# Optimization experiments

Hardware: AMD Instinct MI355X
Metric: run time of the kernel (lower is better)

## Reference

```python
import jax, jax.numpy as jnp
import numpy as np

N, E = 50000, 800000
IN, MID, OUT = 128, 256, 128
LN_EPS = 1e-5


def layer_norm(x, gamma, beta, eps=LN_EPS):
    mu = jnp.mean(x, axis=-1, keepdims=True)
    var = jnp.mean(jnp.square(x - mu), axis=-1, keepdims=True)
    return (x - mu) * jax.lax.rsqrt(var + eps) * gamma + beta


def gcn_conv(x, W, b, src, dst, norm, n):
    # x' = D^{-1/2}(A+I)D^{-1/2} X W + b  (self-loops already folded into src/dst/norm)
    h = x @ W                                  # [N, F_out]
    msg = h[src] * norm[:, None]               # [E+N, F_out] gather + scale
    out = jax.ops.segment_sum(msg, dst, num_segments=n)
    return out + b


def setup_inputs() -> dict:
    key = jax.random.key(0)
    ks = jax.random.split(key, 4)
    x = jax.random.normal(ks[0], (N, IN), dtype=jnp.float32)
    edge_index = jax.random.randint(ks[1], (2, E), 0, N, dtype=jnp.int32)
    W1 = jax.random.normal(ks[2], (IN, MID), dtype=jnp.float32) * (1.0 / np.sqrt(IN))
    b1 = jnp.zeros((MID,), jnp.float32)
    g1 = jnp.ones((IN,), jnp.float32)
    be1 = jnp.zeros((IN,), jnp.float32)
    W4 = jax.random.normal(ks[3], (MID, OUT), dtype=jnp.float32) * (1.0 / np.sqrt(MID))
    b4 = jnp.zeros((OUT,), jnp.float32)
    g4 = jnp.ones((MID,), jnp.float32)
    be4 = jnp.zeros((MID,), jnp.float32)
    return {"x": x, "W1": W1, "b1": b1, "g1": g1, "be1": be1,
            "W4": W4, "b4": b4, "g4": g4, "be4": be4,
            "edge_index": edge_index}


def reference(x, W1, b1, g1, be1, W4, b4, g4, be4, edge_index):
    n = x.shape[0]
    loop = jnp.arange(n, dtype=edge_index.dtype)
    src = jnp.concatenate([edge_index[0], loop])   # [E+N]
    dst = jnp.concatenate([edge_index[1], loop])   # [E+N]
    deg = jax.ops.segment_sum(jnp.ones_like(src, x.dtype), dst, num_segments=n)
    dinv = jax.lax.rsqrt(deg)                      # deg >= 1 thanks to self-loops
    norm = dinv[src] * dinv[dst]                   # [E+N]

    h = gcn_conv(layer_norm(x, g1, be1), W1, b1, src, dst, norm, n)
    h = jax.nn.gelu(h, approximate=False)          # torch F.gelu default = exact erf
    h = gcn_conv(layer_norm(h, g4, be4), W4, b4, src, dst, norm, n)
    return h
```

## Files before the change

### kernel.cpp

```cpp
#include <hip/hip_runtime.h>
#include <math.h>

#define N_NODES 50000
#define E_EDGES 800000

typedef __attribute__((ext_vector_type(4))) float f32x4;
typedef __attribute__((ext_vector_type(8))) short s16x8;

#define T1_OFF    0UL
#define AGG1_OFF  12800000UL
#define T2B_OFF   38400000UL
#define WB1H_OFF  64000000UL
#define WB1L_OFF  64100096UL
#define WB4H_OFF  64200192UL
#define WB4L_OFF  64300288UL
#define DINV_OFF  64400384UL
#define HIST_OFF  64600576UL
#define RP_OFF    64800768UL
#define CUR_OFF   65001088UL
#define CSR_OFF   65201408UL
#define BSUM_OFF  71601408UL

__device__ __forceinline__ float lo16f(unsigned u) { return __uint_as_float(u << 16); }
__device__ __forceinline__ float hi16f(unsigned u) { return __uint_as_float(u & 0xffff0000u); }
__device__ __forceinline__ unsigned pack2bf(float a, float b) {
  unsigned ua = __float_as_uint(a); ua += 0x7fffu + ((ua >> 16) & 1u);
  unsigned ub = __float_as_uint(b); ub += 0x7fffu + ((ub >> 16) & 1u);
  return (ua >> 16) | (ub & 0xffff0000u);
}
__device__ __forceinline__ float gelu_f(float x) {
  return 0.5f * x * (1.f + erff(x * 0.70710678118654752f));
}

__global__ __launch_bounds__(256) void init_hist(int* __restrict__ hist, int n) {
  int i = blockIdx.x * 256 + threadIdx.x;
  if (i < n) hist[i] = 0;
}

__global__ __launch_bounds__(256) void hist_kernel(const int* __restrict__ dst,
                                                   int* __restrict__ hist, int e) {
  int i = blockIdx.x * 256 + threadIdx.x;
  if (i < e) atomicAdd(&hist[dst[i]], 1);
}

__global__ __launch_bounds__(256) void dinv_kernel(const int* __restrict__ hist,
                                                   float* __restrict__ dinv, int n) {
  int i = blockIdx.x * 256 + threadIdx.x;
  if (i < n) dinv[i] = rsqrtf((float)(hist[i] + 1));
}

__global__ __launch_bounds__(1024) void scan_partial(const int* __restrict__ hist,
                                                     int* __restrict__ rp,
                                                     int* __restrict__ bsum, int n) {
  __shared__ int wsum[16];
  int tid = threadIdx.x, lane = tid & 63, wv = tid >> 6;
  int i = blockIdx.x * 1024 + tid;
  int v = (i < n) ? hist[i] : 0;
  int sc = v;
  #pragma unroll
  for (int m = 1; m < 64; m <<= 1) { int o = __shfl_up(sc, m); if (lane >= m) sc += o; }
  if (lane == 63) wsum[wv] = sc;
  __syncthreads();
  if (wv == 0) {
    int w = (lane < 16) ? wsum[lane] : 0;
    int swc = w;
    #pragma unroll
    for (int m = 1; m < 16; m <<= 1) { int o = __shfl_up(swc, m); if (lane >= m) swc += o; }
    if (lane < 16) wsum[lane] = swc - w;
    if (lane == 15) bsum[blockIdx.x] = swc;
  }
  __syncthreads();
  if (i < n) rp[i] = (sc - v) + wsum[wv];
}

__global__ __launch_bounds__(64) void scan_bsums(int* __restrict__ bsum, int nb) {
  int lane = threadIdx.x;
  int v = (lane < nb) ? bsum[lane] : 0;
  int sc = v;
  #pragma unroll
  for (int m = 1; m < 64; m <<= 1) { int o = __shfl_up(sc, m); if (lane >= m) sc += o; }
  if (lane < nb) bsum[lane] = sc - v;
  if (lane == 63) bsum[nb] = sc;
}

__global__ __launch_bounds__(1024) void scan_add(int* __restrict__ rp,
                                                 int* __restrict__ cursor,
                                                 const int* __restrict__ bsum, int n) {
  int i = blockIdx.x * 1024 + threadIdx.x;
  if (i < n) {
    int v = rp[i] + bsum[blockIdx.x];
    rp[i] = v; cursor[i] = v;
  }
  if (i == 0) rp[n] = bsum[gridDim.x];
}

__global__ __launch_bounds__(256) void fill_kernel(const int* __restrict__ src,
                                                   const int* __restrict__ dst,
                                                   const float* __restrict__ dinv,
                                                   int* __restrict__ cursor,
                                                   int2* __restrict__ csr, int e) {
  int i = blockIdx.x * 256 + threadIdx.x;
  if (i < e) {
    int s = src[i], d = dst[i];
    int pos = atomicAdd(&cursor[d], 1);
    csr[pos] = make_int2(s, __float_as_int(dinv[s] * dinv[d]));
  }
}

__global__ __launch_bounds__(256) void convW_split(const float* __restrict__ W,
                                                   unsigned* __restrict__ Wh,
                                                   unsigned* __restrict__ Wl, int K, int N) {
  int tid = blockIdx.x * 256 + threadIdx.x;
  if (tid >= (K * N) / 8) return;
  int c15 = tid & 15;
  int kg  = (tid >> 4) & 3;
  int KS  = K >> 5;
  int ks  = (tid >> 6) % KS;
  int nt  = (tid >> 6) / KS;
  int col = nt * 16 + c15;
  int k0  = ks * 32 + kg * 8;
  float w[8];
  #pragma unroll
  for (int j = 0; j < 8; ++j) w[j] = W[(size_t)(k0 + j) * N + col];
  uint4 h, l;
  h.x = pack2bf(w[0], w[1]); l.x = pack2bf(w[0] - lo16f(h.x), w[1] - hi16f(h.x));
  h.y = pack2bf(w[2], w[3]); l.y = pack2bf(w[2] - lo16f(h.y), w[3] - hi16f(h.y));
  h.z = pack2bf(w[4], w[5]); l.z = pack2bf(w[4] - lo16f(h.z), w[5] - hi16f(h.z));
  h.w = pack2bf(w[6], w[7]); l.w = pack2bf(w[6] - lo16f(h.w), w[7] - hi16f(h.w));
  *reinterpret_cast<uint4*>(Wh + (size_t)tid * 4) = h;
  *reinterpret_cast<uint4*>(Wl + (size_t)tid * 4) = l;
}

__global__ __launch_bounds__(256) void ln1_kernel(const float* __restrict__ x,
                                                  const float* __restrict__ g,
                                                  const float* __restrict__ be,
                                                  unsigned* __restrict__ T) {
  int lane = threadIdx.x & 63, wv = threadIdx.x >> 6;
  int row = blockIdx.x * 4 + wv;
  float2 v = *reinterpret_cast<const float2*>(x + (size_t)row * 128 + lane * 2);
  float s = v.x + v.y, sq = v.x * v.x + v.y * v.y;
  #pragma unroll
  for (int m = 1; m < 64; m <<= 1) { s += __shfl_xor(s, m); sq += __shfl_xor(sq, m); }
  float mu = s * (1.f / 128.f);
  float var = sq * (1.f / 128.f) - mu * mu;
  float rs = rsqrtf(var + 1e-5f);
  float2 gg = *reinterpret_cast<const float2*>(g + lane * 2);
  float2 bb = *reinterpret_cast<const float2*>(be + lane * 2);
  T[(size_t)row * 64 + lane] =
      pack2bf((v.x - mu) * rs * gg.x + bb.x, (v.y - mu) * rs * gg.y + bb.y);
}

template <int MODE>
__global__ __launch_bounds__(256) void agg128(const unsigned* __restrict__ T,
                                              const int* __restrict__ rp,
                                              const int2* __restrict__ csr,
                                              const float* __restrict__ dinv,
                                              const float* __restrict__ b,
                                              void* __restrict__ outv) {
  int lane = threadIdx.x & 63, wv = threadIdx.x >> 6;
  int node = blockIdx.x * 4 + wv;
  float di = dinv[node], sn = di * di;
  unsigned us = T[(size_t)node * 64 + lane];
  float a0 = lo16f(us) * sn, a1 = hi16f(us) * sn;
  int e = rp[node], e1 = rp[node + 1];
  for (; e + 3 < e1; e += 4) {
    int4 ca = *reinterpret_cast<const int4*>(&csr[e]);
    int4 cb = *reinterpret_cast<const int4*>(&csr[e + 2]);
    unsigned u0 = T[(size_t)ca.x * 64 + lane];
    unsigned u1 = T[(size_t)ca.z * 64 + lane];
    unsigned u2 = T[(size_t)cb.x * 64 + lane];
    unsigned u3 = T[(size_t)cb.z * 64 + lane];
    float n0 = __int_as_float(ca.y), n1 = __int_as_float(ca.w);
    float n2 = __int_as_float(cb.y), n3 = __int_as_float(cb.w);
    a0 += lo16f(u0) * n0; a1 += hi16f(u0) * n0;
    a0 += lo16f(u1) * n1; a1 += hi16f(u1) * n1;
    a0 += lo16f(u2) * n2; a1 += hi16f(u2) * n2;
    a0 += lo16f(u3) * n3; a1 += hi16f(u3) * n3;
  }
  for (; e < e1; ++e) {
    int2 c = csr[e];
    unsigned u = T[(size_t)c.x * 64 + lane];
    float nr = __int_as_float(c.y);
    a0 += lo16f(u) * nr; a1 += hi16f(u) * nr;
  }
  if (MODE == 0) {
    *reinterpret_cast<float2*>((float*)outv + (size_t)node * 128 + lane * 2) =
        make_float2(a0, a1);
  } else if (MODE == 1) {
    ((unsigned*)outv)[(size_t)node * 64 + lane] = pack2bf(a0, a1);
  } else {
    float2 bb = *reinterpret_cast<const float2*>(b + lane * 2);
    *reinterpret_cast<float2*>((float*)outv + (size_t)node * 128 + lane * 2) =
        make_float2(a0 + bb.x, a1 + bb.y);
  }
}

__global__ __launch_bounds__(256) void gemm1_fused(const float* __restrict__ A,
                                                   const unsigned* __restrict__ Wh,
                                                   const unsigned* __restrict__ Wl,
                                                   const float* __restrict__ b,
                                                   const float* __restrict__ g,
                                                   const float* __restrict__ be,
                                                   unsigned* __restrict__ T2b, int n) {
  __shared__ float st[32 * 260];
  int t = threadIdx.x, lane = t & 63, w = t >> 6;
  int rtile = (w >> 1) * 16;
  int c0 = (w & 1) * 128;
  int arow = blockIdx.x * 32 + rtile + (lane & 15);
  if (arow >= n) arow = n - 1;
  const float* aptr = A + (size_t)arow * 128 + (lane >> 4) * 8;
  f32x4 acc[8];
  #pragma unroll
  for (int nf = 0; nf < 8; ++nf) acc[nf] = (f32x4)(0.f);
  #pragma unroll
  for (int ks = 0; ks < 4; ++ks) {
    float4 v0 = *reinterpret_cast<const float4*>(aptr + ks * 32);
    float4 v1 = *reinterpret_cast<const float4*>(aptr + ks * 32 + 4);
    uint4 h, l;
    h.x = pack2bf(v0.x, v0.y); l.x = pack2bf(v0.x - lo16f(h.x), v0.y - hi16f(h.x));
    h.y = pack2bf(v0.z, v0.w); l.y = pack2bf(v0.z - lo16f(h.y), v0.w - hi16f(h.y));
    h.z = pack2bf(v1.x, v1.y); l.z = pack2bf(v1.x - lo16f(h.z), v1.y - hi16f(h.z));
    h.w = pack2bf(v1.z, v1.w); l.w = pack2bf(v1.z - lo16f(h.w), v1.w - hi16f(h.w));
    s16x8 ah = *reinterpret_cast<s16x8*>(&h);
    s16x8 al = *reinterpret_cast<s16x8*>(&l);
    #pragma unroll
    for (int nf = 0; nf < 8; ++nf) {
      int nt = (c0 >> 4) + nf;
      size_t bo = (size_t)(((nt * 4 + ks) * 4 + (lane >> 4)) * 16 + (lane & 15)) * 4;
      s16x8 bh = *reinterpret_cast<const s16x8*>(Wh + bo);
      s16x8 bl = *reinterpret_cast<const s16x8*>(Wl + bo);
      acc[nf] = __builtin_amdgcn_mfma_f32_16x16x32_bf16(ah, bh, acc[nf], 0, 0, 0);
      acc[nf] = __builtin_amdgcn_mfma_f32_16x16x32_bf16(al, bh, acc[nf], 0, 0, 0);
      acc[nf] = __builtin_amdgcn_mfma_f32_16x16x32_bf16(ah, bl, acc[nf], 0, 0, 0);
    }
  }
  #pragma unroll
  for (int nf = 0; nf < 8; ++nf) {
    int col = c0 + nf * 16 + (lane & 15);
    float bb = b[col];
    #pragma unroll
    for (int r = 0; r < 4; ++r) {
      int row = rtile + (lane >> 4) * 4 + r;
      st[row * 260 + col] = gelu_f(acc[nf][r] + bb);
    }
  }
  __syncthreads();
  float4 gg = *reinterpret_cast<const float4*>(g + lane * 4);
  float4 bb2 = *reinterpret_cast<const float4*>(be + lane * 4);
  #pragma unroll
  for (int rr = 0; rr < 8; ++rr) {
    int row = w * 8 + rr;
    float4 v = *reinterpret_cast<const float4*>(&st[row * 260 + lane * 4]);
    float s = v.x + v.y + v.z + v.w;
    float sq = v.x * v.x + v.y * v.y + v.z * v.z + v.w * v.w;
    #pragma unroll
    for (int m = 1; m < 64; m <<= 1) { s += __shfl_xor(s, m); sq += __shfl_xor(sq, m); }
    float mu = s * (1.f / 256.f);
    float var = sq * (1.f / 256.f) - mu * mu;
    float rs = rsqrtf(var + 1e-5f);
    int gr = blockIdx.x * 32 + row;
    if (gr < n) {
      uint2 p;
      p.x = pack2bf((v.x - mu) * rs * gg.x + bb2.x, (v.y - mu) * rs * gg.y + bb2.y);
      p.y = pack2bf((v.z - mu) * rs * gg.z + bb2.z, (v.w - mu) * rs * gg.w + bb2.w);
      *reinterpret_cast<uint2*>(T2b + (size_t)gr * 128 + lane * 2) = p;
    }
  }
}

__global__ __launch_bounds__(256) void gemm2_mfma(const unsigned* __restrict__ Ab,
                                                  const unsigned* __restrict__ Wh,
                                                  const unsigned* __restrict__ Wl,
                                                  unsigned* __restrict__ T2, int n) {
  __shared__ float st[32 * 132];
  int t = threadIdx.x, lane = t & 63, w = t >> 6;
  int rtile = (w >> 1) * 16;
  int c0 = (w & 1) * 64;
  int arow = blockIdx.x * 32 + rtile + (lane & 15);
  if (arow >= n) arow = n - 1;
  const unsigned* aptr = Ab + (size_t)arow * 128 + (lane >> 4) * 4;
  f32x4 acc[4];
  #pragma unroll
  for (int nf = 0; nf < 4; ++nf) acc[nf] = (f32x4)(0.f);
  #pragma unroll
  for (int ks = 0; ks < 8; ++ks) {
    s16x8 af = *reinterpret_cast<const s16x8*>(aptr + ks * 16);
    #pragma unroll
    for (int nf = 0; nf < 4; ++nf) {
      int nt = (c0 >> 4) + nf;
      size_t bo = (size_t)(((nt * 8 + ks) * 4 + (lane >> 4)) * 16 + (lane & 15)) * 4;
      s16x8 bh = *reinterpret_cast<const s16x8*>(Wh + bo);
      s16x8 bl = *reinterpret_cast<const s16x8*>(Wl + bo);
      acc[nf] = __builtin_amdgcn_mfma_f32_16x16x32_bf16(af, bh, acc[nf], 0, 0, 0);
      acc[nf] = __builtin_amdgcn_mfma_f32_16x16x32_bf16(af, bl, acc[nf], 0, 0, 0);
    }
  }
  #pragma unroll
  for (int nf = 0; nf < 4; ++nf) {
    int col = c0 + nf * 16 + (lane & 15);
    #pragma unroll
    for (int r = 0; r < 4; ++r) {
      int row = rtile + (lane >> 4) * 4 + r;
      st[row * 132 + col] = acc[nf][r];
    }
  }
  __syncthreads();
  #pragma unroll
  for (int rr = 0; rr < 8; ++rr) {
    int row = w * 8 + rr;
    int gr = blockIdx.x * 32 + row;
    if (gr < n) {
      float2 v = *reinterpret_cast<const float2*>(&st[row * 132 + lane * 2]);
      T2[(size_t)gr * 64 + lane] = pack2bf(v.x, v.y);
    }
  }
}

extern "C" void kernel_launch(void* const* d_in, const int* in_sizes, int n_in,
                              void* d_out, int out_size, void* d_ws, size_t ws_size,
                              hipStream_t stream) {
  (void)in_sizes; (void)n_in; (void)out_size; (void)ws_size;
  const float* x   = (const float*)d_in[0];
  const float* W1  = (const float*)d_in[1];
  const float* b1  = (const float*)d_in[2];
  const float* g1  = (const float*)d_in[3];
  const float* be1 = (const float*)d_in[4];
  const float* W4  = (const float*)d_in[5];
  const float* b4  = (const float*)d_in[6];
  const float* g4  = (const float*)d_in[7];
  const float* be4 = (const float*)d_in[8];
  const int*   ei  = (const int*)d_in[9];
  const int* src = ei;
  const int* dst = ei + E_EDGES;

  char* ws = (char*)d_ws;
  unsigned* T1    = (unsigned*)(ws + T1_OFF);
  unsigned* T2    = (unsigned*)(ws + T1_OFF);
  float*    AGG1  = (float*)(ws + AGG1_OFF);
  unsigned* T2b   = (unsigned*)(ws + T2B_OFF);
  unsigned* Wb1h  = (unsigned*)(ws + WB1H_OFF);
  unsigned* Wb1l  = (unsigned*)(ws + WB1L_OFF);
  unsigned* Wb4h  = (unsigned*)(ws + WB4H_OFF);
  unsigned* Wb4l  = (unsigned*)(ws + WB4L_OFF);
  float* dinv     = (float*)(ws + DINV_OFF);
  int*   hist     = (int*)(ws + HIST_OFF);
  int*   rp       = (int*)(ws + RP_OFF);
  int*   cursor   = (int*)(ws + CUR_OFF);
  int2*  csr      = (int2*)(ws + CSR_OFF);
  int*   bsum     = (int*)(ws + BSUM_OFF);
  float* outp     = (float*)d_out;

  int nblkN = (N_NODES + 255) / 256;
  int nblkE = (E_EDGES + 255) / 256;
  int nbScan = (N_NODES + 1023) / 1024;
  int nblkG = (N_NODES + 31) / 32;

  hipLaunchKernelGGL(init_hist, dim3(nblkN), dim3(256), 0, stream, hist, N_NODES);
  hipLaunchKernelGGL(hist_kernel, dim3(nblkE), dim3(256), 0, stream, dst, hist, E_EDGES);
  hipLaunchKernelGGL(dinv_kernel, dim3(nblkN), dim3(256), 0, stream, hist, dinv, N_NODES);
  hipLaunchKernelGGL(scan_partial, dim3(nbScan), dim3(1024), 0, stream, hist, rp, bsum, N_NODES);
  hipLaunchKernelGGL(scan_bsums, dim3(1), dim3(64), 0, stream, bsum, nbScan);
  hipLaunchKernelGGL(scan_add, dim3(nbScan), dim3(1024), 0, stream, rp, cursor, bsum, N_NODES);
  hipLaunchKernelGGL(fill_kernel, dim3(nblkE), dim3(256), 0, stream,
                     src, dst, dinv, cursor, csr, E_EDGES);
  hipLaunchKernelGGL(convW_split, dim3(16), dim3(256), 0, stream, W1, Wb1h, Wb1l, 128, 256);
  hipLaunchKernelGGL(convW_split, dim3(16), dim3(256), 0, stream, W4, Wb4h, Wb4l, 256, 128);

  hipLaunchKernelGGL(ln1_kernel, dim3(N_NODES / 4), dim3(256), 0, stream, x, g1, be1, T1);
  hipLaunchKernelGGL(agg128<0>, dim3(N_NODES / 4), dim3(256), 0, stream,
                     T1, rp, csr, dinv, (const float*)nullptr, (void*)AGG1);
  hipLaunchKernelGGL(gemm1_fused, dim3(nblkG), dim3(256), 0, stream,
                     AGG1, Wb1h, Wb1l, b1, g4, be4, T2b, N_NODES);

  hipLaunchKernelGGL(gemm2_mfma, dim3(nblkG), dim3(256), 0, stream, T2b, Wb4h, Wb4l, T2, N_NODES);
  hipLaunchKernelGGL(agg128<2>, dim3(N_NODES / 4), dim3(256), 0, stream,
                     T2, rp, csr, dinv, b4, (void*)outp);
}
```

Before: 250.5 us.

## Build CSR with segmented histogram and precomputed positions, store only source indices

Replaces the atomic-cursor CSR fill with a two-pass scheme. Each edge first records its rank within an 8-way segmented per-node counter (segment chosen by block id), which spreads atomic contention. A scan over the 400K segment counts then gives deterministic placement without a second round of atomics. The CSR now stores only source indices, halving edge storage, and the aggregation kernels recompute the normalization from dinv gathers. This adds a larger scan, a posrel buffer and an extra dinv gather per edge in both aggregations.

```diff
diff --git a/kernel.cpp b/kernel.cpp
--- a/kernel.cpp
+++ b/kernel.cpp
@@ -15,11 +15,11 @@
 #define WB4H_OFF  64200192UL
 #define WB4L_OFF  64300288UL
 #define DINV_OFF  64400384UL
-#define HIST_OFF  64600576UL
-#define RP_OFF    64800768UL
-#define CUR_OFF   65001088UL
-#define CSR_OFF   65201408UL
-#define BSUM_OFF  71601408UL
+#define HIST8_OFF 64600384UL
+#define RP8_OFF   66200384UL
+#define POSREL_OFF 67800448UL
+#define CSRS_OFF  71000448UL
+#define BSUM_OFF  74200448UL
 
 __device__ __forceinline__ float lo16f(unsigned u) { return __uint_as_float(u << 16); }
 __device__ __forceinline__ float hi16f(unsigned u) { return __uint_as_float(u & 0xffff0000u); }
@@ -32,21 +32,19 @@
   return 0.5f * x * (1.f + erff(x * 0.70710678118654752f));
 }
 
-__global__ __launch_bounds__(256) void init_hist(int* __restrict__ hist, int n) {
+__global__ __launch_bounds__(256) void zero_hist8(int4* __restrict__ h) {
   int i = blockIdx.x * 256 + threadIdx.x;
-  if (i < n) hist[i] = 0;
-}
-
-__global__ __launch_bounds__(256) void hist_kernel(const int* __restrict__ dst,
-                                                   int* __restrict__ hist, int e) {
-  int i = blockIdx.x * 256 + threadIdx.x;
-  if (i < e) atomicAdd(&hist[dst[i]], 1);
-}
-
-__global__ __launch_bounds__(256) void dinv_kernel(const int* __restrict__ hist,
-                                                   float* __restrict__ dinv, int n) {
-  int i = blockIdx.x * 256 + threadIdx.x;
-  if (i < n) dinv[i] = rsqrtf((float)(hist[i] + 1));
+  if (i < 100000) h[i] = make_int4(0, 0, 0, 0);
+}
+
+__global__ __launch_bounds__(256) void edge_pos(const int* __restrict__ dst,
+                                                int* __restrict__ hist8,
+                                                int* __restrict__ posrel) {
+  int e = blockIdx.x * 256 + threadIdx.x;
+  int d = dst[e];
+  int seg = blockIdx.x & 7;
+  int r = atomicAdd(&hist8[d * 8 + seg], 1);
+  __builtin_nontemporal_store(r, posrel + e);
 }
 
 __global__ __launch_bounds__(1024) void scan_partial(const int* __restrict__ hist,
@@ -75,36 +73,45 @@
 
 __global__ __launch_bounds__(64) void scan_bsums(int* __restrict__ bsum, int nb) {
   int lane = threadIdx.x;
-  int v = (lane < nb) ? bsum[lane] : 0;
-  int sc = v;
-  #pragma unroll
-  for (int m = 1; m < 64; m <<= 1) { int o = __shfl_up(sc, m); if (lane >= m) sc += o; }
-  if (lane < nb) bsum[lane] = sc - v;
-  if (lane == 63) bsum[nb] = sc;
+  int carry = 0;
+  for (int base = 0; base < nb; base += 64) {
+    int i = base + lane;
+    int v = (i < nb) ? bsum[i] : 0;
+    int sc = v;
+    #pragma unroll
+    for (int m = 1; m < 64; m <<= 1) { int o = __shfl_up(sc, m); if (lane >= m) sc += o; }
+    if (i < nb) bsum[i] = carry + sc - v;
+    carry += __shfl(sc, 63);
+  }
+  if (lane == 0) bsum[nb] = carry;
 }
 
 __global__ __launch_bounds__(1024) void scan_add(int* __restrict__ rp,
-                                                 int* __restrict__ cursor,
                                                  const int* __restrict__ bsum, int n) {
   int i = blockIdx.x * 1024 + threadIdx.x;
+  if (i < n) rp[i] += bsum[blockIdx.x];
+  if (i == 0) rp[n] = bsum[gridDim.x];
+}
+
+__global__ __launch_bounds__(256) void dinv_kernel(const int* __restrict__ rp8,
+                                                   float* __restrict__ dinv, int n) {
+  int i = blockIdx.x * 256 + threadIdx.x;
   if (i < n) {
-    int v = rp[i] + bsum[blockIdx.x];
-    rp[i] = v; cursor[i] = v;
-  }
-  if (i == 0) rp[n] = bsum[gridDim.x];
-}
-
-__global__ __launch_bounds__(256) void fill_kernel(const int* __restrict__ src,
-                                                   const int* __restrict__ dst,
-                                                   const float* __restrict__ dinv,
-                                                   int* __restrict__ cursor,
-                                                   int2* __restrict__ csr, int e) {
-  int i = blockIdx.x * 256 + threadIdx.x;
-  if (i < e) {
-    int s = src[i], d = dst[i];
-    int pos = atomicAdd(&cursor[d], 1);
-    csr[pos] = make_int2(s, __float_as_int(dinv[s] * dinv[d]));
-  }
+    int deg = rp8[i * 8 + 8] - rp8[i * 8];
+    dinv[i] = rsqrtf((float)(deg + 1));
+  }
+}
+
+__global__ __launch_bounds__(256) void fill2(const int* __restrict__ src,
+                                             const int* __restrict__ dst,
+                                             const int* __restrict__ rp8,
+                                             const int* __restrict__ posrel,
+                                             int* __restrict__ csr_src) {
+  int e = blockIdx.x * 256 + threadIdx.x;
+  int s = src[e], d = dst[e];
+  int seg = blockIdx.x & 7;
+  int pos = rp8[d * 8 + seg] + posrel[e];
+  __builtin_nontemporal_store(s, csr_src + pos);
 }
 
 __global__ __launch_bounds__(256) void convW_split(const float* __restrict__ W,
@@ -152,45 +159,41 @@
 
 template <int MODE>
 __global__ __launch_bounds__(256) void agg128(const unsigned* __restrict__ T,
-                                              const int* __restrict__ rp,
-                                              const int2* __restrict__ csr,
+                                              const int* __restrict__ rp8,
+                                              const int* __restrict__ csr_src,
                                               const float* __restrict__ dinv,
                                               const float* __restrict__ b,
-                                              void* __restrict__ outv) {
+                                              float* __restrict__ out) {
   int lane = threadIdx.x & 63, wv = threadIdx.x >> 6;
   int node = blockIdx.x * 4 + wv;
   float di = dinv[node], sn = di * di;
   unsigned us = T[(size_t)node * 64 + lane];
   float a0 = lo16f(us) * sn, a1 = hi16f(us) * sn;
-  int e = rp[node], e1 = rp[node + 1];
+  int e = rp8[node * 8], e1 = rp8[node * 8 + 8];
   for (; e + 3 < e1; e += 4) {
-    int4 ca = *reinterpret_cast<const int4*>(&csr[e]);
-    int4 cb = *reinterpret_cast<const int4*>(&csr[e + 2]);
-    unsigned u0 = T[(size_t)ca.x * 64 + lane];
-    unsigned u1 = T[(size_t)ca.z * 64 + lane];
-    unsigned u2 = T[(size_t)cb.x * 64 + lane];
-    unsigned u3 = T[(size_t)cb.z * 64 + lane];
-    float n0 = __int_as_float(ca.y), n1 = __int_as_float(ca.w);
-    float n2 = __int_as_float(cb.y), n3 = __int_as_float(cb.w);
+    int4 c = *reinterpret_cast<const int4*>(csr_src + e);
+    unsigned u0 = T[(size_t)c.x * 64 + lane];
+    unsigned u1 = T[(size_t)c.y * 64 + lane];
+    unsigned u2 = T[(size_t)c.z * 64 + lane];
+    unsigned u3 = T[(size_t)c.w * 64 + lane];
+    float n0 = dinv[c.x] * di, n1 = dinv[c.y] * di;
+    float n2 = dinv[c.z] * di, n3 = dinv[c.w] * di;
     a0 += lo16f(u0) * n0; a1 += hi16f(u0) * n0;
     a0 += lo16f(u1) * n1; a1 += hi16f(u1) * n1;
     a0 += lo16f(u2) * n2; a1 += hi16f(u2) * n2;
     a0 += lo16f(u3) * n3; a1 += hi16f(u3) * n3;
   }
   for (; e < e1; ++e) {
-    int2 c = csr[e];
-    unsigned u = T[(size_t)c.x * 64 + lane];
-    float nr = __int_as_float(c.y);
+    int s = csr_src[e];
+    unsigned u = T[(size_t)s * 64 + lane];
+    float nr = dinv[s] * di;
     a0 += lo16f(u) * nr; a1 += hi16f(u) * nr;
   }
   if (MODE == 0) {
-    *reinterpret_cast<float2*>((float*)outv + (size_t)node * 128 + lane * 2) =
-        make_float2(a0, a1);
-  } else if (MODE == 1) {
-    ((unsigned*)outv)[(size_t)node * 64 + lane] = pack2bf(a0, a1);
+    *reinterpret_cast<float2*>(out + (size_t)node * 128 + lane * 2) = make_float2(a0, a1);
   } else {
     float2 bb = *reinterpret_cast<const float2*>(b + lane * 2);
-    *reinterpret_cast<float2*>((float*)outv + (size_t)node * 128 + lane * 2) =
+    *reinterpret_cast<float2*>(out + (size_t)node * 128 + lane * 2) =
         make_float2(a0 + bb.x, a1 + bb.y);
   }
 }
@@ -343,36 +346,36 @@
   unsigned* Wb4h  = (unsigned*)(ws + WB4H_OFF);
   unsigned* Wb4l  = (unsigned*)(ws + WB4L_OFF);
   float* dinv     = (float*)(ws + DINV_OFF);
-  int*   hist     = (int*)(ws + HIST_OFF);
-  int*   rp       = (int*)(ws + RP_OFF);
-  int*   cursor   = (int*)(ws + CUR_OFF);
-  int2*  csr      = (int2*)(ws + CSR_OFF);
+  int*   hist8    = (int*)(ws + HIST8_OFF);
+  int*   rp8      = (int*)(ws + RP8_OFF);
+  int*   posrel   = (int*)(ws + POSREL_OFF);
+  int*   csr_src  = (int*)(ws + CSRS_OFF);
   int*   bsum     = (int*)(ws + BSUM_OFF);
   float* outp     = (float*)d_out;
 
-  int nblkN = (N_NODES + 255) / 256;
-  int nblkE = (E_EDGES + 255) / 256;
-  int nbScan = (N_NODES + 1023) / 1024;
-  int nblkG = (N_NODES + 31) / 32;
-
-  hipLaunchKernelGGL(init_hist, dim3(nblkN), dim3(256), 0, stream, hist, N_NODES);
-  hipLaunchKernelGGL(hist_kernel, dim3(nblkE), dim3(256), 0, stream, dst, hist, E_EDGES);
-  hipLaunchKernelGGL(dinv_kernel, dim3(nblkN), dim3(256), 0, stream, hist, dinv, N_NODES);
-  hipLaunchKernelGGL(scan_partial, dim3(nbScan), dim3(1024), 0, stream, hist, rp, bsum, N_NODES);
+  const int NSEG = N_NODES * 8;
+  int nblkE  = E_EDGES / 256;
+  int nbScan = (NSEG + 1023) / 1024;
+  int nblkG  = (N_NODES + 31) / 32;
+
+  hipLaunchKernelGGL(zero_hist8, dim3(391), dim3(256), 0, stream, (int4*)hist8);
+  hipLaunchKernelGGL(edge_pos, dim3(nblkE), dim3(256), 0, stream, dst, hist8, posrel);
+  hipLaunchKernelGGL(scan_partial, dim3(nbScan), dim3(1024), 0, stream, hist8, rp8, bsum, NSEG);
   hipLaunchKernelGGL(scan_bsums, dim3(1), dim3(64), 0, stream, bsum, nbScan);
-  hipLaunchKernelGGL(scan_add, dim3(nbScan), dim3(1024), 0, stream, rp, cursor, bsum, N_NODES);
-  hipLaunchKernelGGL(fill_kernel, dim3(nblkE), dim3(256), 0, stream,
-                     src, dst, dinv, cursor, csr, E_EDGES);
+  hipLaunchKernelGGL(scan_add, dim3(nbScan), dim3(1024), 0, stream, rp8, bsum, NSEG);
+  hipLaunchKernelGGL(dinv_kernel, dim3((N_NODES + 255) / 256), dim3(256), 0, stream,
+                     rp8, dinv, N_NODES);
+  hipLaunchKernelGGL(fill2, dim3(nblkE), dim3(256), 0, stream, src, dst, rp8, posrel, csr_src);
   hipLaunchKernelGGL(convW_split, dim3(16), dim3(256), 0, stream, W1, Wb1h, Wb1l, 128, 256);
   hipLaunchKernelGGL(convW_split, dim3(16), dim3(256), 0, stream, W4, Wb4h, Wb4l, 256, 128);
 
   hipLaunchKernelGGL(ln1_kernel, dim3(N_NODES / 4), dim3(256), 0, stream, x, g1, be1, T1);
   hipLaunchKernelGGL(agg128<0>, dim3(N_NODES / 4), dim3(256), 0, stream,
-                     T1, rp, csr, dinv, (const float*)nullptr, (void*)AGG1);
+                     T1, rp8, csr_src, dinv, (const float*)nullptr, AGG1);
   hipLaunchKernelGGL(gemm1_fused, dim3(nblkG), dim3(256), 0, stream,
                      AGG1, Wb1h, Wb1l, b1, g4, be4, T2b, N_NODES);
 
   hipLaunchKernelGGL(gemm2_mfma, dim3(nblkG), dim3(256), 0, stream, T2b, Wb4h, Wb4l, T2, N_NODES);
   hipLaunchKernelGGL(agg128<2>, dim3(N_NODES / 4), dim3(256), 0, stream,
-                     T2, rp, csr, dinv, b4, (void*)outp);
-}
+                     T2, rp8, csr_src, dinv, b4, outp);
+}
```

Measured after the change: 234.0 us. 1.07x faster.
